# Optimization experiments

Measured on AMD Instinct MI355X. Metric: run time of the kernel, lower is better.

The kernel has to match this reference:

```python
import jax, jax.numpy as jnp
import numpy as np

MAX_DISP = 4  # init kwarg maxDisplacement


def setup_inputs() -> dict:
    key = jax.random.key(0)
    k1, k2 = jax.random.split(key)
    F1 = jax.random.normal(k1, (8, 128, 128, 128), dtype=jnp.float32)
    F2 = jax.random.normal(k2, (8, 128, 128, 128), dtype=jnp.float32)
    return {"F1": F1, "F2": F2}


def reference(F1, F2):
    d = MAX_DISP
    B, H, W, C = F1.shape
    # Zero-pad F2 spatially by d on each side (NHWC)
    padded = jnp.pad(F2, ((0, 0), (d, d), (d, d), (0, 0)))
    max_offset = 2 * d + 1
    # For each (dy, dx) shift: channel-mean of F1 * shifted-F2 -> [B,H,W]
    costs = [
        jnp.mean(F1 * padded[:, y:y + H, x:x + W, :], axis=3)
        for y in range(max_offset)
        for x in range(max_offset)
    ]
    cost_volume = jnp.stack(costs, axis=3)  # [B, H, W, max_offset^2]
    return jax.nn.leaky_relu(cost_volume, negative_slope=0.1)
```

## Files before the change

### kernel.cpp

```cpp
#include <hip/hip_runtime.h>
#include <hip/hip_bf16.h>
#include <string.h>

typedef __attribute__((ext_vector_type(8))) short bf16x8;
typedef __attribute__((ext_vector_type(4))) float f32x4;

namespace {
constexpr int B = 8, H = 128, W = 128, C = 128;
constexpr int MO = 9, NOFF = 81;
constexpr int ROWS = 4;
constexpr int WCOLS = 16;
constexpr int F2R = 12;
constexpr int F2S = 32;
constexpr int SREAL = 24;
constexpr int CK = 32;
constexpr int NCH = C / CK;
constexpr int NT = 256;
constexpr int NLD = 9;
constexpr int RSTR = F2S * CK;
}

__device__ inline unsigned bf2pack(float a, float b) {
  __hip_bfloat162 h = __float22bfloat162_rn(float2{a, b});
  unsigned r;
  memcpy(&r, &h, sizeof(r));
  return r;
}

__global__ __launch_bounds__(NT, 3) void costvol_kernel(
    const float* __restrict__ F1, const float* __restrict__ F2,
    float* __restrict__ out)
{
  __shared__ __align__(16) short sF2[2][F2R * RSTR];

  const int lin  = blockIdx.x;
  const int b    = lin & 7;
  const int tile = lin >> 3;
  const int rt   = tile & 31;
  const int wt   = tile >> 5;
  const int h0   = rt * ROWS;
  const int wb0  = wt * WCOLS;

  const int tid  = threadIdx.x;
  const int r    = tid >> 6;
  const int lane = tid & 63;
  const int j    = lane & 15;
  const int kq   = lane >> 4;

  int gofs[NLD]; int lofs[NLD]; unsigned okmask = 0;
#pragma unroll
  for (int it = 0; it < NLD; ++it) {
    const int idx  = tid + it * NT;
    const int kg   = idx & 7;
    const int slot = idx >> 3;
    const int ry   = slot / SREAL;
    const int s    = slot - ry * SREAL;
    const int fy   = h0 - 4 + ry;
    const int fx   = wb0 - 4 + s;
    const bool ok  = ((unsigned)fy < (unsigned)H) && ((unsigned)fx < (unsigned)W);
    okmask |= (unsigned)ok << it;
    gofs[it] = ok ? (((b * H + fy) * W + fx) * C + kg * 4) : 0;
    lofs[it] = (ry * F2S + s) * CK + kg * 4;
  }

  auto stage_load = [&](int ch, float4* ld) {
#pragma unroll
    for (int it = 0; it < NLD; ++it) {
      ld[it] = *reinterpret_cast<const float4*>(F2 + gofs[it] + ch * CK);
    }
    __builtin_amdgcn_sched_barrier(0);
  };
  auto stage_store = [&](int buf, const float4* ld) {
#pragma unroll
    for (int it = 0; it < NLD; ++it) {
      uint2 p;
      p.x = bf2pack(ld[it].x, ld[it].y);
      p.y = bf2pack(ld[it].z, ld[it].w);
      if (!((okmask >> it) & 1u)) { p.x = 0u; p.y = 0u; }
      *reinterpret_cast<uint2*>(&sF2[buf][lofs[it]]) = p;
    }
  };

  f32x4 acc[9][2];
#pragma unroll
  for (int d = 0; d < 9; ++d) { acc[d][0] = {0,0,0,0}; acc[d][1] = {0,0,0,0}; }

  bf16x8 afrag[NCH];
  {
    float4 ld[NLD];
    stage_load(0, ld);
    const float* f1p = F1 + (((size_t)b * H + h0 + r) * W + wb0 + j) * C + kq * 8;
    float4 u[NCH][2];
#pragma unroll
    for (int ch = 0; ch < NCH; ++ch) {
      u[ch][0] = *reinterpret_cast<const float4*>(f1p + ch * CK);
      u[ch][1] = *reinterpret_cast<const float4*>(f1p + ch * CK + 4);
    }
    stage_store(0, ld);
#pragma unroll
    for (int ch = 0; ch < NCH; ++ch) {
      uint4 q;
      q.x = bf2pack(u[ch][0].x, u[ch][0].y);
      q.y = bf2pack(u[ch][0].z, u[ch][0].w);
      q.z = bf2pack(u[ch][1].x, u[ch][1].y);
      q.w = bf2pack(u[ch][1].z, u[ch][1].w);
      afrag[ch] = __builtin_bit_cast(bf16x8, q);
    }
    __syncthreads();
  }

#pragma unroll
  for (int ch = 0; ch < NCH; ++ch) {
    float4 ld[NLD];
    if (ch + 1 < NCH) stage_load(ch + 1, ld);

    const short* base = &sF2[ch & 1][(r * F2S + j) * CK + kq * 8];
#pragma unroll
    for (int dy = 0; dy < 9; ++dy) {
      const bf16x8 b0 = *reinterpret_cast<const bf16x8*>(base + dy * RSTR);
      const bf16x8 b1 = *reinterpret_cast<const bf16x8*>(base + dy * RSTR + 16 * CK);
      acc[dy][0] = __builtin_amdgcn_mfma_f32_16x16x32_bf16(afrag[ch], b0, acc[dy][0], 0, 0, 0);
      acc[dy][1] = __builtin_amdgcn_mfma_f32_16x16x32_bf16(afrag[ch], b1, acc[dy][1], 0, 0, 0);
    }

    if (ch + 1 < NCH) {
      __builtin_amdgcn_sched_barrier(0);
      stage_store((ch + 1) & 1, ld);
      __syncthreads();
    }
  }

  const int h = h0 + r;
  float* outb = out + (((size_t)b * H + h) * W + wb0) * NOFF;
#pragma unroll
  for (int dy = 0; dy < 9; ++dy) {
#pragma unroll
    for (int t = 0; t < 2; ++t) {
#pragma unroll
      for (int reg = 0; reg < 4; ++reg) {
        const int i   = kq * 4 + reg;
        const int dxi = j + t * 16 - i;
        if (dxi >= 0 && dxi <= 8) {
          float m = acc[dy][t][reg] * 0.0078125f;
          m = (m > 0.f) ? m : 0.1f * m;
          outb[(size_t)i * NOFF + dy * MO + dxi] = m;
        }
      }
    }
  }
}

extern "C" void kernel_launch(void* const* d_in, const int* in_sizes, int n_in,
                              void* d_out, int out_size, void* d_ws, size_t ws_size,
                              hipStream_t stream) {
  const float* F1 = (const float*)d_in[0];
  const float* F2 = (const float*)d_in[1];
  float* out = (float*)d_out;
  dim3 grid(B * (H / ROWS) * (W / WCOLS));
  dim3 block(NT);
  hipLaunchKernelGGL(costvol_kernel, grid, block, 0, stream, F1, F2, out);
}
```

Measured before the change: 44.92 us.

## Reorganize waves by F2 row with shared F1 fragments and phased channel order

Each wave now owns a residue class of F2 rows and loads each F2 row fragment once, applying it to every output row that needs it. This replaces per-wave dy iteration, which re-read overlapping F2 rows from LDS. F1 is staged pre-scaled by 1/C into LDS so any wave can pull any row's A fragment. Channel chunks are visited in a tile-dependent phase to spread DRAM accesses. Padding zeros are written once, F2S shrinks to 24, and MFMA sections get raised wave priority. In exchange it adds LDS traffic for A fragments, more LDS use, and a four-way template switch.

```diff
diff --git a/kernel.cpp b/kernel.cpp
--- a/kernel.cpp
+++ b/kernel.cpp
@@ -11,13 +11,14 @@
 constexpr int ROWS = 4;
 constexpr int WCOLS = 16;
 constexpr int F2R = 12;
-constexpr int F2S = 32;
+constexpr int F2S = 24;
 constexpr int SREAL = 24;
 constexpr int CK = 32;
 constexpr int NCH = C / CK;
 constexpr int NT = 256;
 constexpr int NLD = 9;
 constexpr int RSTR = F2S * CK;
+constexpr int F2BUF = F2R * RSTR;
 }
 
 __device__ inline unsigned bf2pack(float a, float b) {
@@ -27,11 +28,109 @@
   return r;
 }
 
+__device__ __forceinline__ f32x4 mfma16(bf16x8 a, bf16x8 b, f32x4 c) {
+  return __builtin_amdgcn_mfma_f32_16x16x32_bf16(a, b, c, 0, 0, 0);
+}
+
+template <int OM>
+__device__ __forceinline__ void compute_body(
+    const float* __restrict__ F2, float* __restrict__ out,
+    short* sF2, const short* sF1,
+    const int* gofs, const int* lofs, unsigned okm,
+    int b, int h0, int wb0, int j, int kq, int phase)
+{
+  f32x4 acc[9][2];
+#pragma unroll
+  for (int s = 0; s < 9; ++s) { acc[s][0] = {0,0,0,0}; acc[s][1] = {0,0,0,0}; }
+
+#pragma unroll
+  for (int lc = 0; lc < NCH; ++lc) {
+    float4 ld[NLD];
+    if (lc + 1 < NCH) {
+      const int nach = (lc + 1 + phase) & 3;
+#pragma unroll
+      for (int it = 0; it < NLD; ++it) {
+        ld[it] = *reinterpret_cast<const float4*>(F2 + gofs[it] + nach * CK);
+      }
+      __builtin_amdgcn_sched_barrier(0);
+    }
+    const int ach = (lc + phase) & 3;
+
+    bf16x8 a[4];
+#pragma unroll
+    for (int r = 0; r < 4; ++r) {
+      a[r] = *reinterpret_cast<const bf16x8*>(
+          sF1 + ((r * 4 + ach) * 64 + j * 4 + kq) * 8);
+    }
+
+    const short* bbase = sF2 + (lc & 1) * F2BUF + j * CK + kq * 8;
+    __builtin_amdgcn_s_setprio(1);
+    int slot = 0;
+#pragma unroll
+    for (int rr = 0; rr < 3; ++rr) {
+      const int ry = OM + rr * 4;
+      const bf16x8 b0 = *reinterpret_cast<const bf16x8*>(bbase + ry * RSTR);
+      const bf16x8 b1 = *reinterpret_cast<const bf16x8*>(bbase + ry * RSTR + 16 * CK);
+      const int rlo = (rr == 2) ? OM : 0;
+      const int rhi = (rr == 0) ? OM : 3;
+#pragma unroll
+      for (int r = rlo; r <= rhi; ++r) {
+        acc[slot][0] = mfma16(a[r], b0, acc[slot][0]);
+        acc[slot][1] = mfma16(a[r], b1, acc[slot][1]);
+        ++slot;
+      }
+    }
+    __builtin_amdgcn_s_setprio(0);
+
+    if (lc + 1 < NCH) {
+      __builtin_amdgcn_sched_barrier(0);
+#pragma unroll
+      for (int it = 0; it < NLD; ++it) {
+        if ((okm >> it) & 1u) {
+          uint2 p;
+          p.x = bf2pack(ld[it].x, ld[it].y);
+          p.y = bf2pack(ld[it].z, ld[it].w);
+          *reinterpret_cast<uint2*>(&sF2[((lc + 1) & 1) * F2BUF + lofs[it]]) = p;
+        }
+      }
+      __syncthreads();
+    }
+  }
+
+  int slot = 0;
+#pragma unroll
+  for (int rr = 0; rr < 3; ++rr) {
+    const int ry = OM + rr * 4;
+    const int rlo = (rr == 2) ? OM : 0;
+    const int rhi = (rr == 0) ? OM : 3;
+#pragma unroll
+    for (int r = rlo; r <= rhi; ++r) {
+      const int dy = ry - r;
+      float* outb = out + (((size_t)b * H + h0 + r) * W + wb0) * NOFF + dy * MO;
+#pragma unroll
+      for (int t = 0; t < 2; ++t) {
+#pragma unroll
+        for (int reg = 0; reg < 4; ++reg) {
+          const int i = kq * 4 + reg;
+          const int dxi = j + t * 16 - i;
+          if (dxi >= 0 && dxi <= 8) {
+            float m = acc[slot][t][reg];
+            m = fmaxf(m, 0.1f * m);
+            outb[(size_t)i * NOFF + dxi] = m;
+          }
+        }
+      }
+      ++slot;
+    }
+  }
+}
+
 __global__ __launch_bounds__(NT, 3) void costvol_kernel(
     const float* __restrict__ F1, const float* __restrict__ F2,
     float* __restrict__ out)
 {
-  __shared__ __align__(16) short sF2[2][F2R * RSTR];
+  __shared__ __align__(16) short sF2[2 * F2BUF];
+  __shared__ __align__(16) short sF1[4 * 4 * 64 * 8];
 
   const int lin  = blockIdx.x;
   const int b    = lin & 7;
@@ -40,14 +139,15 @@
   const int wt   = tile >> 5;
   const int h0   = rt * ROWS;
   const int wb0  = wt * WCOLS;
+  const int phase = tile & 3;
 
   const int tid  = threadIdx.x;
-  const int r    = tid >> 6;
+  const int wv   = tid >> 6;
   const int lane = tid & 63;
   const int j    = lane & 15;
   const int kq   = lane >> 4;
 
-  int gofs[NLD]; int lofs[NLD]; unsigned okmask = 0;
+  int gofs[NLD]; int lofs[NLD]; unsigned okm = 0;
 #pragma unroll
   for (int it = 0; it < NLD; ++it) {
     const int idx  = tid + it * NT;
@@ -58,95 +158,63 @@
     const int fy   = h0 - 4 + ry;
     const int fx   = wb0 - 4 + s;
     const bool ok  = ((unsigned)fy < (unsigned)H) && ((unsigned)fx < (unsigned)W);
-    okmask |= (unsigned)ok << it;
+    okm |= (unsigned)ok << it;
     gofs[it] = ok ? (((b * H + fy) * W + fx) * C + kg * 4) : 0;
     lofs[it] = (ry * F2S + s) * CK + kg * 4;
   }
 
-  auto stage_load = [&](int ch, float4* ld) {
-#pragma unroll
-    for (int it = 0; it < NLD; ++it) {
-      ld[it] = *reinterpret_cast<const float4*>(F2 + gofs[it] + ch * CK);
-    }
-    __builtin_amdgcn_sched_barrier(0);
-  };
-  auto stage_store = [&](int buf, const float4* ld) {
-#pragma unroll
-    for (int it = 0; it < NLD; ++it) {
-      uint2 p;
-      p.x = bf2pack(ld[it].x, ld[it].y);
-      p.y = bf2pack(ld[it].z, ld[it].w);
-      if (!((okmask >> it) & 1u)) { p.x = 0u; p.y = 0u; }
-      *reinterpret_cast<uint2*>(&sF2[buf][lofs[it]]) = p;
-    }
-  };
-
-  f32x4 acc[9][2];
-#pragma unroll
-  for (int d = 0; d < 9; ++d) { acc[d][0] = {0,0,0,0}; acc[d][1] = {0,0,0,0}; }
-
-  bf16x8 afrag[NCH];
   {
     float4 ld[NLD];
-    stage_load(0, ld);
-    const float* f1p = F1 + (((size_t)b * H + h0 + r) * W + wb0 + j) * C + kq * 8;
-    float4 u[NCH][2];
-#pragma unroll
-    for (int ch = 0; ch < NCH; ++ch) {
-      u[ch][0] = *reinterpret_cast<const float4*>(f1p + ch * CK);
-      u[ch][1] = *reinterpret_cast<const float4*>(f1p + ch * CK + 4);
-    }
-    stage_store(0, ld);
-#pragma unroll
-    for (int ch = 0; ch < NCH; ++ch) {
+#pragma unroll
+    for (int it = 0; it < NLD; ++it) {
+      ld[it] = *reinterpret_cast<const float4*>(F2 + gofs[it] + phase * CK);
+    }
+    __builtin_amdgcn_sched_barrier(0);
+
+    const int fr  = tid >> 6;
+    const int fpx = (tid >> 2) & 15;
+    const int fcg = tid & 3;
+    const float* f1p =
+        F1 + (((size_t)b * H + h0 + fr) * W + wb0 + fpx) * C + fcg * 32;
+    float4 u[8];
+#pragma unroll
+    for (int q = 0; q < 8; ++q) u[q] = *reinterpret_cast<const float4*>(f1p + q * 4);
+
+#pragma unroll
+    for (int it = 0; it < NLD; ++it) {
+      if (!((okm >> it) & 1u)) {
+        *reinterpret_cast<uint2*>(&sF2[lofs[it]]) = uint2{0u, 0u};
+        *reinterpret_cast<uint2*>(&sF2[F2BUF + lofs[it]]) = uint2{0u, 0u};
+      }
+    }
+#pragma unroll
+    for (int it = 0; it < NLD; ++it) {
+      if ((okm >> it) & 1u) {
+        uint2 p;
+        p.x = bf2pack(ld[it].x, ld[it].y);
+        p.y = bf2pack(ld[it].z, ld[it].w);
+        *reinterpret_cast<uint2*>(&sF2[lofs[it]]) = p;
+      }
+    }
+    constexpr float S = 0.0078125f;
+#pragma unroll
+    for (int kqq = 0; kqq < 4; ++kqq) {
       uint4 q;
-      q.x = bf2pack(u[ch][0].x, u[ch][0].y);
-      q.y = bf2pack(u[ch][0].z, u[ch][0].w);
-      q.z = bf2pack(u[ch][1].x, u[ch][1].y);
-      q.w = bf2pack(u[ch][1].z, u[ch][1].w);
-      afrag[ch] = __builtin_bit_cast(bf16x8, q);
+      q.x = bf2pack(u[2 * kqq].x * S, u[2 * kqq].y * S);
+      q.y = bf2pack(u[2 * kqq].z * S, u[2 * kqq].w * S);
+      q.z = bf2pack(u[2 * kqq + 1].x * S, u[2 * kqq + 1].y * S);
+      q.w = bf2pack(u[2 * kqq + 1].z * S, u[2 * kqq + 1].w * S);
+      *reinterpret_cast<uint4*>(
+          &sF1[((fr * 4 + fcg) * 64 + fpx * 4 + kqq) * 8]) = q;
     }
     __syncthreads();
   }
 
-#pragma unroll
-  for (int ch = 0; ch < NCH; ++ch) {
-    float4 ld[NLD];
-    if (ch + 1 < NCH) stage_load(ch + 1, ld);
-
-    const short* base = &sF2[ch & 1][(r * F2S + j) * CK + kq * 8];
-#pragma unroll
-    for (int dy = 0; dy < 9; ++dy) {
-      const bf16x8 b0 = *reinterpret_cast<const bf16x8*>(base + dy * RSTR);
-      const bf16x8 b1 = *reinterpret_cast<const bf16x8*>(base + dy * RSTR + 16 * CK);
-      acc[dy][0] = __builtin_amdgcn_mfma_f32_16x16x32_bf16(afrag[ch], b0, acc[dy][0], 0, 0, 0);
-      acc[dy][1] = __builtin_amdgcn_mfma_f32_16x16x32_bf16(afrag[ch], b1, acc[dy][1], 0, 0, 0);
-    }
-
-    if (ch + 1 < NCH) {
-      __builtin_amdgcn_sched_barrier(0);
-      stage_store((ch + 1) & 1, ld);
-      __syncthreads();
-    }
-  }
-
-  const int h = h0 + r;
-  float* outb = out + (((size_t)b * H + h) * W + wb0) * NOFF;
-#pragma unroll
-  for (int dy = 0; dy < 9; ++dy) {
-#pragma unroll
-    for (int t = 0; t < 2; ++t) {
-#pragma unroll
-      for (int reg = 0; reg < 4; ++reg) {
-        const int i   = kq * 4 + reg;
-        const int dxi = j + t * 16 - i;
-        if (dxi >= 0 && dxi <= 8) {
-          float m = acc[dy][t][reg] * 0.0078125f;
-          m = (m > 0.f) ? m : 0.1f * m;
-          outb[(size_t)i * NOFF + dy * MO + dxi] = m;
-        }
-      }
-    }
+  switch (wv) {
+    case 0: compute_body<0>(F2, out, sF2, sF1, gofs, lofs, okm, b, h0, wb0, j, kq, phase); break;
+    case 1: compute_body<1>(F2, out, sF2, sF1, gofs, lofs, okm, b, h0, wb0, j, kq, phase); break;
+    case 2: compute_body<2>(F2, out, sF2, sF1, gofs, lofs, okm, b, h0, wb0, j, kq, phase); break;
+    default: compute_body<3>(F2, out, sF2, sF1, gofs, lofs, okm, b, h0, wb0, j, kq, phase); break;
   }
 }
 
```

After: 48.32 us. 7.6% more time.

## Enlarge row tile to 8 rows with 512 threads and deepen F2 prefetch

Applied to the files above, without the earlier changes.

Each block now computes 8 output rows with 512 threads instead of 4 rows with 256. This cuts the redundant F2 halo loaded per block from 3x to 2x, and the shared-memory row stride shrinks to 24 columns plus a small overflow pad. The channel loop is unrolled by hand with two global loads in flight. Out-of-bounds zeros are written once up front instead of on every stage, and the leaky ReLU uses fmaxf. In exchange each block uses more registers and shared memory, and there are fewer blocks (1024), which may lower occupancy or leave wave scheduling less balanced.

```diff
diff --git a/kernel.cpp b/kernel.cpp
--- a/kernel.cpp
+++ b/kernel.cpp
@@ -8,16 +8,17 @@
 namespace {
 constexpr int B = 8, H = 128, W = 128, C = 128;
 constexpr int MO = 9, NOFF = 81;
-constexpr int ROWS = 4;
+constexpr int ROWS = 8;
 constexpr int WCOLS = 16;
-constexpr int F2R = 12;
-constexpr int F2S = 32;
+constexpr int F2R = 16;
+constexpr int F2S = 24;
 constexpr int SREAL = 24;
 constexpr int CK = 32;
 constexpr int NCH = C / CK;
-constexpr int NT = 256;
-constexpr int NLD = 9;
+constexpr int NT = 512;
+constexpr int NLD = 6;
 constexpr int RSTR = F2S * CK;
+constexpr int F2BUF = F2R * RSTR;
 }
 
 __device__ inline unsigned bf2pack(float a, float b) {
@@ -27,17 +28,21 @@
   return r;
 }
 
+__device__ __forceinline__ f32x4 mfma16(bf16x8 a, bf16x8 b, f32x4 c) {
+  return __builtin_amdgcn_mfma_f32_16x16x32_bf16(a, b, c, 0, 0, 0);
+}
+
 __global__ __launch_bounds__(NT, 3) void costvol_kernel(
     const float* __restrict__ F1, const float* __restrict__ F2,
     float* __restrict__ out)
 {
-  __shared__ __align__(16) short sF2[2][F2R * RSTR];
+  __shared__ __align__(16) short sF2[2 * F2BUF + 512];
 
   const int lin  = blockIdx.x;
   const int b    = lin & 7;
   const int tile = lin >> 3;
-  const int rt   = tile & 31;
-  const int wt   = tile >> 5;
+  const int rt   = tile & 15;
+  const int wt   = tile >> 4;
   const int h0   = rt * ROWS;
   const int wb0  = wt * WCOLS;
 
@@ -47,7 +52,7 @@
   const int j    = lane & 15;
   const int kq   = lane >> 4;
 
-  int gofs[NLD]; int lofs[NLD]; unsigned okmask = 0;
+  int gofs[NLD]; int lofs[NLD]; unsigned okm = 0;
 #pragma unroll
   for (int it = 0; it < NLD; ++it) {
     const int idx  = tid + it * NT;
@@ -58,26 +63,27 @@
     const int fy   = h0 - 4 + ry;
     const int fx   = wb0 - 4 + s;
     const bool ok  = ((unsigned)fy < (unsigned)H) && ((unsigned)fx < (unsigned)W);
-    okmask |= (unsigned)ok << it;
+    okm |= (unsigned)ok << it;
     gofs[it] = ok ? (((b * H + fy) * W + fx) * C + kg * 4) : 0;
     lofs[it] = (ry * F2S + s) * CK + kg * 4;
   }
 
-  auto stage_load = [&](int ch, float4* ld) {
+  auto issue = [&](int ch, float4* ld) {
 #pragma unroll
     for (int it = 0; it < NLD; ++it) {
       ld[it] = *reinterpret_cast<const float4*>(F2 + gofs[it] + ch * CK);
     }
     __builtin_amdgcn_sched_barrier(0);
   };
-  auto stage_store = [&](int buf, const float4* ld) {
+  auto pack = [&](int buf, const float4* ld) {
 #pragma unroll
     for (int it = 0; it < NLD; ++it) {
-      uint2 p;
-      p.x = bf2pack(ld[it].x, ld[it].y);
-      p.y = bf2pack(ld[it].z, ld[it].w);
-      if (!((okmask >> it) & 1u)) { p.x = 0u; p.y = 0u; }
-      *reinterpret_cast<uint2*>(&sF2[buf][lofs[it]]) = p;
+      if ((okm >> it) & 1u) {
+        uint2 p;
+        p.x = bf2pack(ld[it].x, ld[it].y);
+        p.y = bf2pack(ld[it].z, ld[it].w);
+        *reinterpret_cast<uint2*>(&sF2[buf * F2BUF + lofs[it]]) = p;
+      }
     }
   };
 
@@ -85,50 +91,65 @@
 #pragma unroll
   for (int d = 0; d < 9; ++d) { acc[d][0] = {0,0,0,0}; acc[d][1] = {0,0,0,0}; }
 
-  bf16x8 afrag[NCH];
+  auto compute = [&](int buf, bf16x8 af) {
+    const short* bbase = &sF2[buf * F2BUF + j * CK + kq * 8];
+#pragma unroll
+    for (int dy = 0; dy < 9; ++dy) {
+      const int ry = r + dy;
+      const bf16x8 b0 = *reinterpret_cast<const bf16x8*>(bbase + ry * RSTR);
+      const bf16x8 b1 = *reinterpret_cast<const bf16x8*>(bbase + ry * RSTR + 16 * CK);
+      acc[dy][0] = mfma16(af, b0, acc[dy][0]);
+      acc[dy][1] = mfma16(af, b1, acc[dy][1]);
+    }
+  };
+
+  bf16x8 a[NCH];
+  float4 ldA[NLD], ldB[NLD];
+  issue(0, ldA);
+  issue(1, ldB);
   {
-    float4 ld[NLD];
-    stage_load(0, ld);
     const float* f1p = F1 + (((size_t)b * H + h0 + r) * W + wb0 + j) * C + kq * 8;
-    float4 u[NCH][2];
+    float4 u0[NCH], u1[NCH];
 #pragma unroll
     for (int ch = 0; ch < NCH; ++ch) {
-      u[ch][0] = *reinterpret_cast<const float4*>(f1p + ch * CK);
-      u[ch][1] = *reinterpret_cast<const float4*>(f1p + ch * CK + 4);
+      u0[ch] = *reinterpret_cast<const float4*>(f1p + ch * CK);
+      u1[ch] = *reinterpret_cast<const float4*>(f1p + ch * CK + 4);
     }
-    stage_store(0, ld);
+#pragma unroll
+    for (int it = 0; it < NLD; ++it) {
+      if (!((okm >> it) & 1u)) {
+        *reinterpret_cast<uint2*>(&sF2[lofs[it]]) = uint2{0u, 0u};
+        *reinterpret_cast<uint2*>(&sF2[F2BUF + lofs[it]]) = uint2{0u, 0u};
+      }
+    }
+    pack(0, ldA);
 #pragma unroll
     for (int ch = 0; ch < NCH; ++ch) {
       uint4 q;
-      q.x = bf2pack(u[ch][0].x, u[ch][0].y);
-      q.y = bf2pack(u[ch][0].z, u[ch][0].w);
-      q.z = bf2pack(u[ch][1].x, u[ch][1].y);
-      q.w = bf2pack(u[ch][1].z, u[ch][1].w);
-      afrag[ch] = __builtin_bit_cast(bf16x8, q);
+      q.x = bf2pack(u0[ch].x, u0[ch].y);
+      q.y = bf2pack(u0[ch].z, u0[ch].w);
+      q.z = bf2pack(u1[ch].x, u1[ch].y);
+      q.w = bf2pack(u1[ch].z, u1[ch].w);
+      a[ch] = __builtin_bit_cast(bf16x8, q);
     }
     __syncthreads();
   }
 
-#pragma unroll
-  for (int ch = 0; ch < NCH; ++ch) {
-    float4 ld[NLD];
-    if (ch + 1 < NCH) stage_load(ch + 1, ld);
-
-    const short* base = &sF2[ch & 1][(r * F2S + j) * CK + kq * 8];
-#pragma unroll
-    for (int dy = 0; dy < 9; ++dy) {
-      const bf16x8 b0 = *reinterpret_cast<const bf16x8*>(base + dy * RSTR);
-      const bf16x8 b1 = *reinterpret_cast<const bf16x8*>(base + dy * RSTR + 16 * CK);
-      acc[dy][0] = __builtin_amdgcn_mfma_f32_16x16x32_bf16(afrag[ch], b0, acc[dy][0], 0, 0, 0);
-      acc[dy][1] = __builtin_amdgcn_mfma_f32_16x16x32_bf16(afrag[ch], b1, acc[dy][1], 0, 0, 0);
-    }
-
-    if (ch + 1 < NCH) {
-      __builtin_amdgcn_sched_barrier(0);
-      stage_store((ch + 1) & 1, ld);
-      __syncthreads();
-    }
-  }
+  issue(2, ldA);
+  compute(0, a[0]);
+  __builtin_amdgcn_sched_barrier(0);
+  pack(1, ldB);
+  __syncthreads();
+  issue(3, ldB);
+  compute(1, a[1]);
+  __builtin_amdgcn_sched_barrier(0);
+  pack(0, ldA);
+  __syncthreads();
+  compute(0, a[2]);
+  __builtin_amdgcn_sched_barrier(0);
+  pack(1, ldB);
+  __syncthreads();
+  compute(1, a[3]);
 
   const int h = h0 + r;
   float* outb = out + (((size_t)b * H + h) * W + wb0) * NOFF;
@@ -142,7 +163,7 @@
         const int dxi = j + t * 16 - i;
         if (dxi >= 0 && dxi <= 8) {
           float m = acc[dy][t][reg] * 0.0078125f;
-          m = (m > 0.f) ? m : 0.1f * m;
+          m = fmaxf(m, 0.1f * m);
           outb[(size_t)i * NOFF + dy * MO + dxi] = m;
         }
       }
```

Measured after the change: 57.57 us. 1.28x slower.
